# Optimization experiments

Hardware: AMD Instinct MI355X
Metric: run time of the kernel (lower is better)

## Reference

```python
import jax, jax.numpy as jnp
import numpy as np

SQ, B, NH, HN = 2048, 2, 16, 128
LAYER_NUM = 1  # coeff; net scale = coeff / (sqrt(HN)*coeff) = 1/sqrt(HN)
MASK_FILL = -10000.0


def setup_inputs() -> dict:
    key = jax.random.key(0)
    kq, kk, kv = jax.random.split(key, 3)
    q = jax.random.normal(kq, (SQ, B, NH, HN), dtype=jnp.float32)
    k = jax.random.normal(kk, (SQ, B, NH, HN), dtype=jnp.float32)
    v = jax.random.normal(kv, (SQ, B, NH, HN), dtype=jnp.float32)
    # causal mask: True where attention is NOT allowed (strictly upper triangular)
    mask = jnp.triu(jnp.ones((SQ, SQ), dtype=bool), k=1)[None, None]
    return {"query_layer": q, "key_layer": k, "value_layer": v, "attention_mask": mask}


def reference(query_layer, key_layer, value_layer, attention_mask):
    sq, b, nh, hn = query_layer.shape
    coeff = float(LAYER_NUM)
    norm_factor = jnp.sqrt(jnp.float32(hn)) * coeff
    # baddbmm QK^T with alpha=1/norm_factor, then FusedScaleMaskSoftmax scale=coeff
    scores = jnp.einsum("sbhd,tbhd->bhst", query_layer, key_layer) * (coeff / norm_factor)
    scores = jnp.where(attention_mask, jnp.float32(MASK_FILL), scores)
    probs = jax.nn.softmax(scores, axis=-1)
    # dropout (p=0.1) treated as identity (eval / deterministic reference)
    ctx = jnp.einsum("bhst,tbhd->sbhd", probs, value_layer)  # [sq,b,nh,hn]
    return ctx.reshape(sq, b, nh * hn)
```

## Files before the change

kernel.cpp:

```cpp
#include <hip/hip_runtime.h>
#include <hip/hip_bf16.h>

#define SQi  2048
#define SBHi 4096
#define SCALE 0.08838834764831845f
#define PP   72

typedef __attribute__((ext_vector_type(4))) float f32x4;
typedef __attribute__((ext_vector_type(8))) short bf16x8;

__device__ __forceinline__ short f2bf(float f) {
    union { float f; unsigned u; } v; v.f = f;
    unsigned r = v.u + 0x7fffu + ((v.u >> 16) & 1u);
    return (short)(r >> 16);
}

__global__ __launch_bounds__(256)
void conv_kf(const float* __restrict__ K, short* __restrict__ KF) {
    const int g = (int)blockIdx.x * 256 + (int)threadIdx.x;
    const int lane = g & 63, kk = (g >> 6) & 3, t16 = (g >> 8) & 127, bh = g >> 15;
    const int s = t16 * 16 + (lane & 15);
    const int d = kk * 32 + (lane >> 4) * 8;
    const float* in = K + (size_t)s * SBHi + (size_t)(bh >> 4) * 2048 + (bh & 15) * 128 + d;
    f32x4 a = *(const f32x4*)in;
    f32x4 b = *(const f32x4*)(in + 4);
    bf16x8 h;
    #pragma unroll
    for (int i = 0; i < 4; ++i) { h[i] = f2bf(a[i]); h[4 + i] = f2bf(b[i]); }
    *(bf16x8*)(KF + (size_t)g * 8) = h;
}

__global__ __launch_bounds__(256)
void conv_vf(const float* __restrict__ V, short* __restrict__ VF) {
    const int g = (int)blockIdx.x * 256 + (int)threadIdx.x;
    const int lane = g & 63, nn = (g >> 6) & 7, t32 = (g >> 9) & 63, bh = g >> 15;
    const int s = t32 * 32 + (lane >> 4) * 8;
    const int d = nn * 16 + (lane & 15);
    const float* in = V + (size_t)s * SBHi + (size_t)(bh >> 4) * 2048 + (bh & 15) * 128 + d;
    bf16x8 h;
    #pragma unroll
    for (int e = 0; e < 8; ++e) h[e] = f2bf(in[(size_t)e * SBHi]);
    *(bf16x8*)(VF + (size_t)g * 8) = h;
}

__global__ __launch_bounds__(256)
void attn_fwd3(const float* __restrict__ Q, const short* __restrict__ KF,
               const short* __restrict__ VF, float* __restrict__ O) {
    __shared__ __align__(16) short P_lds[4][16 * PP];

    const int bid = (int)blockIdx.x;
    const int xcd = bid & 7, j = bid >> 3;
    const int bh  = xcd + 8 * (j >> 4);
    const int pr  = j & 15;

    const size_t bh_q = (size_t)(bh >> 4) * 2048 + (size_t)(bh & 15) * 128;
    const short* KFb = KF + (size_t)bh * 262144;
    const short* VFb = VF + (size_t)bh * 262144;

    const int t = (int)threadIdx.x;
    const int lane = t & 63, wv = t >> 6, l15 = lane & 15, lhi = lane >> 4;

    for (int half = 0; half < 2; ++half) {
        const int qt = half ? (31 - pr) : pr;

        bf16x8 q_frag[4];
        {
            const int qrow = qt * 64 + wv * 16 + l15;
            const float* qp = Q + (size_t)qrow * SBHi + bh_q + lhi * 8;
            #pragma unroll
            for (int kk = 0; kk < 4; ++kk) {
                f32x4 a = *(const f32x4*)(qp + kk * 32);
                f32x4 b = *(const f32x4*)(qp + kk * 32 + 4);
                #pragma unroll
                for (int i = 0; i < 4; ++i) {
                    q_frag[kk][i]     = f2bf(a[i] * SCALE);
                    q_frag[kk][4 + i] = f2bf(b[i] * SCALE);
                }
            }
        }

        float m_r[4], l_part[4];
        #pragma unroll
        for (int r = 0; r < 4; ++r) { m_r[r] = -1e30f; l_part[r] = 0.f; }
        f32x4 o_acc[8];
        #pragma unroll
        for (int nn = 0; nn < 8; ++nn) o_acc[nn] = (f32x4){0.f, 0.f, 0.f, 0.f};

        const int row0 = qt * 64 + wv * 16 + lhi * 4;

        for (int it = 0; it <= qt; ++it) {
            f32x4 s_acc[4];
            #pragma unroll
            for (int kb = 0; kb < 4; ++kb) s_acc[kb] = (f32x4){0.f, 0.f, 0.f, 0.f};
            const short* kbase = KFb + (size_t)it * 8192 + lane * 8;
            #pragma unroll
            for (int kb = 0; kb < 4; ++kb) {
                #pragma unroll
                for (int kk = 0; kk < 4; ++kk) {
                    bf16x8 kfr = *(const bf16x8*)(kbase + (kb * 4 + kk) * 512);
                    s_acc[kb] = __builtin_amdgcn_mfma_f32_16x16x32_bf16(q_frag[kk], kfr, s_acc[kb], 0, 0, 0);
                }
            }

            bf16x8 vfr0[8], vfr1[8];
            const short* vbase = VFb + (size_t)it * 8192 + lane * 8;
            #pragma unroll
            for (int nn = 0; nn < 8; ++nn) {
                vfr0[nn] = *(const bf16x8*)(vbase + nn * 512);
                vfr1[nn] = *(const bf16x8*)(vbase + (8 + nn) * 512);
            }

            const bool need_mask = (it == qt);

            #pragma unroll
            for (int r = 0; r < 4; ++r) {
                const int rg = row0 + r;
                float s0 = s_acc[0][r];
                float s1 = s_acc[1][r];
                float s2 = s_acc[2][r];
                float s3 = s_acc[3][r];
                if (need_mask) {
                    const int c = it * 64 + l15;
                    if (c      > rg) s0 = -1e30f;
                    if (c + 16 > rg) s1 = -1e30f;
                    if (c + 32 > rg) s2 = -1e30f;
                    if (c + 48 > rg) s3 = -1e30f;
                }
                float mx = fmaxf(fmaxf(s0, s1), fmaxf(s2, s3));
                #pragma unroll
                for (int m = 1; m < 16; m <<= 1) mx = fmaxf(mx, __shfl_xor(mx, m));
                if (mx > m_r[r] + 8.f) {
                    const float corr = __expf(m_r[r] - mx);
                    m_r[r] = mx;
                    l_part[r] *= corr;
                    #pragma unroll
                    for (int nn = 0; nn < 8; ++nn) o_acc[nn][r] *= corr;
                }
                const float mm = m_r[r];
                const float p0 = __expf(s0 - mm);
                const float p1 = __expf(s1 - mm);
                const float p2 = __expf(s2 - mm);
                const float p3 = __expf(s3 - mm);
                l_part[r] += (p0 + p1) + (p2 + p3);
                const int rl = (lhi * 4 + r) * PP;
                P_lds[wv][rl + l15]      = f2bf(p0);
                P_lds[wv][rl + 16 + l15] = f2bf(p1);
                P_lds[wv][rl + 32 + l15] = f2bf(p2);
                P_lds[wv][rl + 48 + l15] = f2bf(p3);
            }

            bf16x8 pa0 = *(const bf16x8*)&P_lds[wv][l15 * PP + lhi * 8];
            bf16x8 pa1 = *(const bf16x8*)&P_lds[wv][l15 * PP + 32 + lhi * 8];
            #pragma unroll
            for (int nn = 0; nn < 8; ++nn) {
                o_acc[nn] = __builtin_amdgcn_mfma_f32_16x16x32_bf16(pa0, vfr0[nn], o_acc[nn], 0, 0, 0);
                o_acc[nn] = __builtin_amdgcn_mfma_f32_16x16x32_bf16(pa1, vfr1[nn], o_acc[nn], 0, 0, 0);
            }
        }

        #pragma unroll
        for (int r = 0; r < 4; ++r) {
            float ls = l_part[r];
            #pragma unroll
            for (int m = 1; m < 16; m <<= 1) ls += __shfl_xor(ls, m);
            const float inv = 1.0f / ls;
            float* op = O + (size_t)(row0 + r) * SBHi + bh_q + l15;
            #pragma unroll
            for (int nn = 0; nn < 8; ++nn) op[nn * 16] = o_acc[nn][r] * inv;
        }
    }
}

extern "C" void kernel_launch(void* const* d_in, const int* in_sizes, int n_in,
                              void* d_out, int out_size, void* d_ws, size_t ws_size,
                              hipStream_t stream) {
    const float* q = (const float*)d_in[0];
    const float* k = (const float*)d_in[1];
    const float* v = (const float*)d_in[2];
    float* out = (float*)d_out;

    short* KF = (short*)d_ws;
    short* VF = KF + (size_t)32 * 262144;

    conv_kf<<<4096, 256, 0, stream>>>(k, KF);
    conv_vf<<<4096, 256, 0, stream>>>(v, VF);
    attn_fwd3<<<512, 256, 0, stream>>>(q, KF, VF, out);
}
```

Before: 107.5 us.

## Repartition causal attention work per wave, fuse K/V conversion kernels

```diff
diff --git a/kernel.cpp b/kernel.cpp
--- a/kernel.cpp
+++ b/kernel.cpp
@@ -10,48 +10,47 @@
 typedef __attribute__((ext_vector_type(8))) short bf16x8;
 
 __device__ __forceinline__ short f2bf(float f) {
-    union { float f; unsigned u; } v; v.f = f;
-    unsigned r = v.u + 0x7fffu + ((v.u >> 16) & 1u);
-    return (short)(r >> 16);
+    __hip_bfloat16 h = __float2bfloat16(f);
+    return *reinterpret_cast<short*>(&h);
 }
 
 __global__ __launch_bounds__(256)
-void conv_kf(const float* __restrict__ K, short* __restrict__ KF) {
-    const int g = (int)blockIdx.x * 256 + (int)threadIdx.x;
-    const int lane = g & 63, kk = (g >> 6) & 3, t16 = (g >> 8) & 127, bh = g >> 15;
-    const int s = t16 * 16 + (lane & 15);
-    const int d = kk * 32 + (lane >> 4) * 8;
-    const float* in = K + (size_t)s * SBHi + (size_t)(bh >> 4) * 2048 + (bh & 15) * 128 + d;
-    f32x4 a = *(const f32x4*)in;
-    f32x4 b = *(const f32x4*)(in + 4);
-    bf16x8 h;
-    #pragma unroll
-    for (int i = 0; i < 4; ++i) { h[i] = f2bf(a[i]); h[4 + i] = f2bf(b[i]); }
-    *(bf16x8*)(KF + (size_t)g * 8) = h;
+void conv_kv(const float* __restrict__ K, const float* __restrict__ V,
+             short* __restrict__ KF, short* __restrict__ VF) {
+    int g = (int)blockIdx.x * 256 + (int)threadIdx.x;
+    if (g < (1 << 20)) {
+        const int lane = g & 63, kk = (g >> 6) & 3, t16 = (g >> 8) & 127, bh = g >> 15;
+        const int s = t16 * 16 + (lane & 15);
+        const int d = kk * 32 + (lane >> 4) * 8;
+        const float* in = K + (size_t)s * SBHi + (size_t)(bh >> 4) * 2048 + (bh & 15) * 128 + d;
+        f32x4 a = *(const f32x4*)in;
+        f32x4 b = *(const f32x4*)(in + 4);
+        bf16x8 h;
+        #pragma unroll
+        for (int i = 0; i < 4; ++i) { h[i] = f2bf(a[i]); h[4 + i] = f2bf(b[i]); }
+        *(bf16x8*)(KF + (size_t)g * 8) = h;
+    } else {
+        g -= (1 << 20);
+        const int lane = g & 63, nn = (g >> 6) & 7, t32 = (g >> 9) & 63, bh = g >> 15;
+        const int s = t32 * 32 + (lane >> 4) * 8;
+        const int d = nn * 16 + (lane & 15);
+        const float* in = V + (size_t)s * SBHi + (size_t)(bh >> 4) * 2048 + (bh & 15) * 128 + d;
+        bf16x8 h;
+        #pragma unroll
+        for (int e = 0; e < 8; ++e) h[e] = f2bf(in[(size_t)e * SBHi]);
+        *(bf16x8*)(VF + (size_t)g * 8) = h;
+    }
 }
 
-__global__ __launch_bounds__(256)
-void conv_vf(const float* __restrict__ V, short* __restrict__ VF) {
-    const int g = (int)blockIdx.x * 256 + (int)threadIdx.x;
-    const int lane = g & 63, nn = (g >> 6) & 7, t32 = (g >> 9) & 63, bh = g >> 15;
-    const int s = t32 * 32 + (lane >> 4) * 8;
-    const int d = nn * 16 + (lane & 15);
-    const float* in = V + (size_t)s * SBHi + (size_t)(bh >> 4) * 2048 + (bh & 15) * 128 + d;
-    bf16x8 h;
-    #pragma unroll
-    for (int e = 0; e < 8; ++e) h[e] = f2bf(in[(size_t)e * SBHi]);
-    *(bf16x8*)(VF + (size_t)g * 8) = h;
-}
-
-__global__ __launch_bounds__(256)
-void attn_fwd3(const float* __restrict__ Q, const short* __restrict__ KF,
+__global__ __launch_bounds__(256, 4)
+void attn_fwd4(const float* __restrict__ Q, const short* __restrict__ KF,
                const short* __restrict__ VF, float* __restrict__ O) {
     __shared__ __align__(16) short P_lds[4][16 * PP];
 
     const int bid = (int)blockIdx.x;
     const int xcd = bid & 7, j = bid >> 3;
-    const int bh  = xcd + 8 * (j >> 4);
-    const int pr  = j & 15;
+    const int bh  = xcd + 8 * (j >> 5);
+    const int p   = j & 31;
 
     const size_t bh_q = (size_t)(bh >> 4) * 2048 + (size_t)(bh & 15) * 128;
     const short* KFb = KF + (size_t)bh * 262144;
@@ -60,114 +59,114 @@
     const int t = (int)threadIdx.x;
     const int lane = t & 63, wv = t >> 6, l15 = lane & 15, lhi = lane >> 4;
 
-    for (int half = 0; half < 2; ++half) {
-        const int qt = half ? (31 - pr) : pr;
+    const int qt32  = (wv < 2) ? p : 63 - p;
+    const int row0w = qt32 * 32 + (wv & 1) * 16;
+    const int dt    = (row0w + 15) >> 6;
 
-        bf16x8 q_frag[4];
-        {
-            const int qrow = qt * 64 + wv * 16 + l15;
-            const float* qp = Q + (size_t)qrow * SBHi + bh_q + lhi * 8;
+    bf16x8 q_frag[4];
+    {
+        const float* qp = Q + (size_t)(row0w + l15) * SBHi + bh_q + lhi * 8;
+        #pragma unroll
+        for (int kk = 0; kk < 4; ++kk) {
+            f32x4 a = *(const f32x4*)(qp + kk * 32);
+            f32x4 b = *(const f32x4*)(qp + kk * 32 + 4);
+            #pragma unroll
+            for (int i = 0; i < 4; ++i) {
+                q_frag[kk][i]     = f2bf(a[i] * SCALE);
+                q_frag[kk][4 + i] = f2bf(b[i] * SCALE);
+            }
+        }
+    }
+
+    float m_r[4], l_part[4];
+    #pragma unroll
+    for (int r = 0; r < 4; ++r) { m_r[r] = -1e30f; l_part[r] = 0.f; }
+    f32x4 o_acc[8];
+    #pragma unroll
+    for (int nn = 0; nn < 8; ++nn) o_acc[nn] = (f32x4){0.f, 0.f, 0.f, 0.f};
+
+    const int row0 = row0w + lhi * 4;
+
+    for (int it = 0; it <= dt; ++it) {
+        f32x4 s_acc[4];
+        #pragma unroll
+        for (int kb = 0; kb < 4; ++kb) s_acc[kb] = (f32x4){0.f, 0.f, 0.f, 0.f};
+        const short* kbase = KFb + (size_t)it * 8192 + lane * 8;
+        #pragma unroll
+        for (int kb = 0; kb < 4; ++kb) {
             #pragma unroll
             for (int kk = 0; kk < 4; ++kk) {
-                f32x4 a = *(const f32x4*)(qp + kk * 32);
-                f32x4 b = *(const f32x4*)(qp + kk * 32 + 4);
-                #pragma unroll
-                for (int i = 0; i < 4; ++i) {
-                    q_frag[kk][i]     = f2bf(a[i] * SCALE);
-                    q_frag[kk][4 + i] = f2bf(b[i] * SCALE);
-                }
+                bf16x8 kfr = *(const bf16x8*)(kbase + (kb * 4 + kk) * 512);
+                s_acc[kb] = __builtin_amdgcn_mfma_f32_16x16x32_bf16(q_frag[kk], kfr, s_acc[kb], 0, 0, 0);
             }
         }
 
-        float m_r[4], l_part[4];
+        const short* vbase = VFb + (size_t)it * 8192 + lane * 8;
+        bf16x8 vfr0[8];
         #pragma unroll
-        for (int r = 0; r < 4; ++r) { m_r[r] = -1e30f; l_part[r] = 0.f; }
-        f32x4 o_acc[8];
-        #pragma unroll
-        for (int nn = 0; nn < 8; ++nn) o_acc[nn] = (f32x4){0.f, 0.f, 0.f, 0.f};
+        for (int nn = 0; nn < 8; ++nn) vfr0[nn] = *(const bf16x8*)(vbase + nn * 512);
 
-        const int row0 = qt * 64 + wv * 16 + lhi * 4;
-
-        for (int it = 0; it <= qt; ++it) {
-            f32x4 s_acc[4];
-            #pragma unroll
-            for (int kb = 0; kb < 4; ++kb) s_acc[kb] = (f32x4){0.f, 0.f, 0.f, 0.f};
-            const short* kbase = KFb + (size_t)it * 8192 + lane * 8;
-            #pragma unroll
-            for (int kb = 0; kb < 4; ++kb) {
-                #pragma unroll
-                for (int kk = 0; kk < 4; ++kk) {
-                    bf16x8 kfr = *(const bf16x8*)(kbase + (kb * 4 + kk) * 512);
-                    s_acc[kb] = __builtin_amdgcn_mfma_f32_16x16x32_bf16(q_frag[kk], kfr, s_acc[kb], 0, 0, 0);
-                }
-            }
-
-            bf16x8 vfr0[8], vfr1[8];
-            const short* vbase = VFb + (size_t)it * 8192 + lane * 8;
-            #pragma unroll
-            for (int nn = 0; nn < 8; ++nn) {
-                vfr0[nn] = *(const bf16x8*)(vbase + nn * 512);
-                vfr1[nn] = *(const bf16x8*)(vbase + (8 + nn) * 512);
-            }
-
-            const bool need_mask = (it == qt);
-
-            #pragma unroll
-            for (int r = 0; r < 4; ++r) {
-                const int rg = row0 + r;
-                float s0 = s_acc[0][r];
-                float s1 = s_acc[1][r];
-                float s2 = s_acc[2][r];
-                float s3 = s_acc[3][r];
-                if (need_mask) {
-                    const int c = it * 64 + l15;
-                    if (c      > rg) s0 = -1e30f;
-                    if (c + 16 > rg) s1 = -1e30f;
-                    if (c + 32 > rg) s2 = -1e30f;
-                    if (c + 48 > rg) s3 = -1e30f;
-                }
-                float mx = fmaxf(fmaxf(s0, s1), fmaxf(s2, s3));
-                #pragma unroll
-                for (int m = 1; m < 16; m <<= 1) mx = fmaxf(mx, __shfl_xor(mx, m));
-                if (mx > m_r[r] + 8.f) {
-                    const float corr = __expf(m_r[r] - mx);
-                    m_r[r] = mx;
-                    l_part[r] *= corr;
-                    #pragma unroll
-                    for (int nn = 0; nn < 8; ++nn) o_acc[nn][r] *= corr;
-                }
-                const float mm = m_r[r];
-                const float p0 = __expf(s0 - mm);
-                const float p1 = __expf(s1 - mm);
-                const float p2 = __expf(s2 - mm);
-                const float p3 = __expf(s3 - mm);
-                l_part[r] += (p0 + p1) + (p2 + p3);
-                const int rl = (lhi * 4 + r) * PP;
-                P_lds[wv][rl + l15]      = f2bf(p0);
-                P_lds[wv][rl + 16 + l15] = f2bf(p1);
-                P_lds[wv][rl + 32 + l15] = f2bf(p2);
-                P_lds[wv][rl + 48 + l15] = f2bf(p3);
-            }
-
-            bf16x8 pa0 = *(const bf16x8*)&P_lds[wv][l15 * PP + lhi * 8];
-            bf16x8 pa1 = *(const bf16x8*)&P_lds[wv][l15 * PP + 32 + lhi * 8];
-            #pragma unroll
-            for (int nn = 0; nn < 8; ++nn) {
-                o_acc[nn] = __builtin_amdgcn_mfma_f32_16x16x32_bf16(pa0, vfr0[nn], o_acc[nn], 0, 0, 0);
-                o_acc[nn] = __builtin_amdgcn_mfma_f32_16x16x32_bf16(pa1, vfr1[nn], o_acc[nn], 0, 0, 0);
-            }
-        }
+        const bool need_mask = (it == dt);
 
         #pragma unroll
         for (int r = 0; r < 4; ++r) {
-            float ls = l_part[r];
+            const int rg = row0 + r;
+            float s0 = s_acc[0][r];
+            float s1 = s_acc[1][r];
+            float s2 = s_acc[2][r];
+            float s3 = s_acc[3][r];
+            if (need_mask) {
+                const int c = it * 64 + l15;
+                if (c      > rg) s0 = -1e30f;
+                if (c + 16 > rg) s1 = -1e30f;
+                if (c + 32 > rg) s2 = -1e30f;
+                if (c + 48 > rg) s3 = -1e30f;
+            }
+            float mx = fmaxf(fmaxf(s0, s1), fmaxf(s2, s3));
             #pragma unroll
-            for (int m = 1; m < 16; m <<= 1) ls += __shfl_xor(ls, m);
-            const float inv = 1.0f / ls;
-            float* op = O + (size_t)(row0 + r) * SBHi + bh_q + l15;
-            #pragma unroll
-            for (int nn = 0; nn < 8; ++nn) op[nn * 16] = o_acc[nn][r] * inv;
+            for (int m = 1; m < 16; m <<= 1) mx = fmaxf(mx, __shfl_xor(mx, m));
+            if (mx > m_r[r] + 8.f) {
+                const float corr = __expf(m_r[r] - mx);
+                m_r[r] = mx;
+                l_part[r] *= corr;
+                #pragma unroll
+                for (int nn = 0; nn < 8; ++nn) o_acc[nn][r] *= corr;
+            }
+            const float mm = m_r[r];
+            const float p0 = __expf(s0 - mm);
+            const float p1 = __expf(s1 - mm);
+            const float p2 = __expf(s2 - mm);
+            const float p3 = __expf(s3 - mm);
+            l_part[r] += (p0 + p1) + (p2 + p3);
+            const int rl = (lhi * 4 + r) * PP;
+            P_lds[wv][rl + l15]      = f2bf(p0);
+            P_lds[wv][rl + 16 + l15] = f2bf(p1);
+            P_lds[wv][rl + 32 + l15] = f2bf(p2);
+            P_lds[wv][rl + 48 + l15] = f2bf(p3);
         }
+
+        bf16x8 pa0 = *(const bf16x8*)&P_lds[wv][l15 * PP + lhi * 8];
+        bf16x8 pa1 = *(const bf16x8*)&P_lds[wv][l15 * PP + 32 + lhi * 8];
+        bf16x8 vfr1[8];
+        #pragma unroll
+        for (int nn = 0; nn < 8; ++nn) vfr1[nn] = *(const bf16x8*)(vbase + (8 + nn) * 512);
+        #pragma unroll
+        for (int nn = 0; nn < 8; ++nn)
+            o_acc[nn] = __builtin_amdgcn_mfma_f32_16x16x32_bf16(pa0, vfr0[nn], o_acc[nn], 0, 0, 0);
+        #pragma unroll
+        for (int nn = 0; nn < 8; ++nn)
+            o_acc[nn] = __builtin_amdgcn_mfma_f32_16x16x32_bf16(pa1, vfr1[nn], o_acc[nn], 0, 0, 0);
+    }
+
+    #pragma unroll
+    for (int r = 0; r < 4; ++r) {
+        float ls = l_part[r];
+        #pragma unroll
+        for (int m = 1; m < 16; m <<= 1) ls += __shfl_xor(ls, m);
+        const float inv = 1.0f / ls;
+        float* op = O + (size_t)(row0 + r) * SBHi + bh_q + l15;
+        #pragma unroll
+        for (int nn = 0; nn < 8; ++nn) op[nn * 16] = o_acc[nn][r] * inv;
     }
 }
 
@@ -182,7 +181,6 @@
     short* KF = (short*)d_ws;
     short* VF = KF + (size_t)32 * 262144;
 
-    conv_kf<<<4096, 256, 0, stream>>>(k, KF);
-    conv_vf<<<4096, 256, 0, stream>>>(v, VF);
-    attn_fwd3<<<512, 256, 0, stream>>>(q, KF, VF, out);
+    conv_kv<<<8192, 256, 0, stream>>>(k, v, KF, VF);
+    attn_fwd4<<<1024, 256, 0, stream>>>(q, KF, VF, out);
 }
```

Measured after the change: 154.7 us. 43.9% more time.
